# Kernel optimization log

Hardware: AMD Instinct MI355X
Metric: run time of the kernel (lower is better)

## Reference

```python
import jax, jax.numpy as jnp
import numpy as np

DIM = 1024
HEADS = 16
DIM_HEAD = 64
INNER = HEADS * DIM_HEAD  # 1024
SCALE = DIM_HEAD ** -0.5


def setup_inputs() -> dict:
    key = jax.random.key(0)
    k_x, k_qkv, k_out, k_g, k_b = jax.random.split(key, 5)
    x = jax.random.normal(k_x, (4, 2048, DIM), dtype=jnp.float32)
    # LayerNorm affine params (torch default: weight=1, bias=0; keep learnable-shaped)
    ln_gamma = jnp.ones((DIM,), dtype=jnp.float32)
    ln_beta = jnp.zeros((DIM,), dtype=jnp.float32)
    w_qkv = jax.random.normal(k_qkv, (DIM, 3 * INNER), dtype=jnp.float32) * (DIM ** -0.5)
    w_out = jax.random.normal(k_out, (INNER, DIM), dtype=jnp.float32) * (INNER ** -0.5)
    return {"x": x, "ln_gamma": ln_gamma, "ln_beta": ln_beta, "w_qkv": w_qkv, "w_out": w_out}


def reference(x, ln_gamma, ln_beta, w_qkv, w_out):
    # LayerNorm (eps matches torch default 1e-5)
    mu = jnp.mean(x, axis=-1, keepdims=True)
    var = jnp.mean(jnp.square(x - mu), axis=-1, keepdims=True)
    xn = (x - mu) * jax.lax.rsqrt(var + 1e-5) * ln_gamma + ln_beta

    qkv = xn @ w_qkv  # [b, n, 3*inner]
    q, k, v = jnp.split(qkv, 3, axis=-1)

    def to_heads(t):  # b n (h d) -> b h n d
        b, n, _ = t.shape
        return t.reshape(b, n, HEADS, DIM_HEAD).transpose(0, 2, 1, 3)

    q, k, v = to_heads(q), to_heads(k), to_heads(v)

    dots = jnp.einsum('bhid,bhjd->bhij', q, k) * SCALE  # [b,h,n,n]
    attn = jax.nn.softmax(dots, axis=-1)
    out = jnp.einsum('bhij,bhjd->bhid', attn, v)  # [b,h,n,d]

    b, h, n, d = out.shape
    out = out.transpose(0, 2, 1, 3).reshape(b, n, h * d)  # b h n d -> b n (h d)
    return out @ w_out
```

## Files before the change

### kernel.cpp

```cpp
#include <hip/hip_runtime.h>

#define DIM 1024
#define HEADS 16
#define DHEAD 64
#define SEQ 2048
#define BATCH 4
#define ROWS (BATCH*SEQ)
#define QK_COLS (3*DIM)
#define QSCALE 0.18033688011112042f

typedef __bf16 bf16x8 __attribute__((ext_vector_type(8)));
typedef __bf16 bf16x4 __attribute__((ext_vector_type(4)));
typedef short s16x4 __attribute__((ext_vector_type(4)));
typedef float f32x4 __attribute__((ext_vector_type(4)));
typedef unsigned short u16;
typedef unsigned int u32;

__device__ __forceinline__ u16 f2bf(float f) {
  u32 u = __float_as_uint(f);
  u = (u + 0x7fffu + ((u >> 16) & 1u)) >> 16;
  return (u16)u;
}

__device__ __forceinline__ void gld16(const void* g, void* s) {
  __builtin_amdgcn_global_load_lds((__attribute__((address_space(1))) void*)g,
                                   (__attribute__((address_space(3))) void*)s, 16, 0, 0);
}

__device__ __forceinline__ float fexp2(float x) {
#if defined(__HIP_DEVICE_COMPILE__)
  return __builtin_amdgcn_exp2f(x);
#else
  return x;
#endif
}

__device__ __forceinline__ f32x4 mfma16(s16x4 a, s16x4 b, f32x4 c) {
#if defined(__HIP_DEVICE_COMPILE__)
  return __builtin_amdgcn_mfma_f32_16x16x16bf16_1k(a, b, c, 0, 0, 0);
#else
  return c;
#endif
}

__device__ __forceinline__ s16x4 pack_bf16(f32x4 v) {
  bf16x4 b = __builtin_convertvector(v, bf16x4);
  union { bf16x4 b; s16x4 s; } u; u.b = b; return u.s;
}

__global__ __launch_bounds__(256) void ln_kernel(const float* __restrict__ x,
    const float* __restrict__ gam, const float* __restrict__ bet, u16* __restrict__ xn) {
  int row = blockIdx.x, tid = threadIdx.x;
  int lane = tid & 63, w = tid >> 6;
  const float4 xv = *(const float4*)(x + (size_t)row*DIM + tid*4);
  float s = xv.x + xv.y + xv.z + xv.w;
  float q = xv.x*xv.x + xv.y*xv.y + xv.z*xv.z + xv.w*xv.w;
  for (int off = 32; off > 0; off >>= 1) { s += __shfl_xor(s, off, 64); q += __shfl_xor(q, off, 64); }
  __shared__ float red[8];
  if (lane == 0) { red[w] = s; red[4+w] = q; }
  __syncthreads();
  s = red[0]+red[1]+red[2]+red[3];
  q = red[4]+red[5]+red[6]+red[7];
  float mean = s * (1.0f/DIM);
  float rstd = rsqrtf(q*(1.0f/DIM) - mean*mean + 1e-5f);
  float4 gv = *(const float4*)(gam + tid*4);
  float4 bv = *(const float4*)(bet + tid*4);
  ushort4 o;
  o.x = f2bf((xv.x-mean)*rstd*gv.x + bv.x);
  o.y = f2bf((xv.y-mean)*rstd*gv.y + bv.y);
  o.z = f2bf((xv.z-mean)*rstd*gv.z + bv.z);
  o.w = f2bf((xv.w-mean)*rstd*gv.w + bv.w);
  *(ushort4*)(xn + (size_t)row*DIM + tid*4) = o;
}

__global__ __launch_bounds__(256) void transpose_w(const float* __restrict__ in,
    u16* __restrict__ out, int R, int C) {
  __shared__ float tile[32][33];
  int c0 = blockIdx.x * 32, r0 = blockIdx.y * 32;
  int tx = threadIdx.x & 31, ty = threadIdx.x >> 5;
  for (int i = 0; i < 32; i += 8)
    tile[ty+i][tx] = in[(size_t)(r0+ty+i)*C + c0 + tx];
  __syncthreads();
  for (int i = 0; i < 32; i += 8)
    out[(size_t)(c0+ty+i)*R + r0 + tx] = f2bf(tile[tx][ty+i]);
}

template<int NOUT, int EPI>
__global__ __launch_bounds__(256, 2) void gemm_bt(const u16* __restrict__ A, const u16* __restrict__ Bt,
                                                  void* __restrict__ Cv, u16* __restrict__ vT, int K) {
  __shared__ alignas(16) u16 As[128*32];
  __shared__ alignas(16) u16 Bs[128*32];
  int tid = threadIdx.x;
  int lane = tid & 63, w = tid >> 6;
  int l = lane & 15, quad = lane >> 4;
  int wm = (w & 1) * 64, wn = (w >> 1) * 64;
  int m0 = blockIdx.y * 128, n0 = blockIdx.x * 128;
  const u16* Ag = A + (size_t)m0 * K;
  const u16* Bg = Bt + (size_t)n0 * K;
  bool sw = (EPI == 1) || (n0 < 2048);
  f32x4 z = {0.f, 0.f, 0.f, 0.f};
  f32x4 acc[4][4];
  for (int i = 0; i < 4; ++i) for (int j = 0; j < 4; ++j) acc[i][j] = z;
  for (int kt = 0; kt < K; kt += 32) {
    __syncthreads();
    for (int c = 0; c < 2; ++c) {
      int idx = c*256 + tid;
      int row = idx >> 2, col = (idx & 3) << 3;
      gld16(Ag + (size_t)row*K + kt + col, (u16*)As + idx*8);
      gld16(Bg + (size_t)row*K + kt + col, (u16*)Bs + idx*8);
    }
    __syncthreads();
    bf16x8 af[4], bfr[4];
    for (int t = 0; t < 4; ++t) {
      af[t]  = *(const bf16x8*)(As + (wm + t*16 + l)*32 + quad*8);
      bfr[t] = *(const bf16x8*)(Bs + (wn + t*16 + l)*32 + quad*8);
    }
    if (sw) {
      for (int i = 0; i < 4; ++i)
        for (int j = 0; j < 4; ++j)
          acc[i][j] = __builtin_amdgcn_mfma_f32_16x16x32_bf16(bfr[i], af[j], acc[i][j], 0, 0, 0);
    } else {
      for (int i = 0; i < 4; ++i)
        for (int j = 0; j < 4; ++j)
          acc[i][j] = __builtin_amdgcn_mfma_f32_16x16x32_bf16(af[i], bfr[j], acc[i][j], 0, 0, 0);
    }
  }
  if (EPI == 0) {
    u16* C = (u16*)Cv;
    int region = n0 >> 10;
    if (region == 0) {
      for (int i = 0; i < 4; ++i)
        for (int j = 0; j < 4; ++j) {
          int nq = n0 + wn + i*16 + quad*4;
          int m  = m0 + wm + j*16 + l;
          f32x4 v = acc[i][j] * QSCALE;
          *(s16x4*)(C + (size_t)m*QK_COLS + nq) = pack_bf16(v);
        }
    } else if (region == 1) {
      for (int i = 0; i < 4; ++i)
        for (int j = 0; j < 4; ++j) {
          int nq = n0 + wn + i*16 + quad*4;
          int m  = m0 + wm + j*16 + l;
          int d  = nq & 63;
          int col = (nq & ~63) | ((((d >> 3) ^ (m & 7)) << 3) | (d & 7));
          *(s16x4*)(C + (size_t)m*QK_COLS + col) = pack_bf16(acc[i][j]);
        }
    } else {
      for (int i = 0; i < 4; ++i)
        for (int j = 0; j < 4; ++j) {
          int mrow = m0 + wm + i*16 + quad*4;
          int hd   = (n0 - 2048) + wn + j*16 + l;
          int h = hd >> 6, d = hd & 63;
          int bb = mrow >> 11, nloc = mrow & 2047;
          int c = nloc >> 2;
          int cs = (c & ~31) | ((c & 31) ^ (d & 31));
          *(s16x4*)(vT + ((size_t)(bb*16 + h)*DHEAD + d)*SEQ + cs*4) = pack_bf16(acc[i][j]);
        }
    }
  } else {
    float* C = (float*)Cv;
    for (int i = 0; i < 4; ++i)
      for (int j = 0; j < 4; ++j) {
        int n = n0 + wn + i*16 + quad*4;
        int m = m0 + wm + j*16 + l;
        *(f32x4*)(C + (size_t)m*NOUT + n) = acc[i][j];
      }
  }
}

__global__ __launch_bounds__(256, 2) void attn_kernel(const u16* __restrict__ qkv,
    const u16* __restrict__ vT, u16* __restrict__ aout) {
  __shared__ alignas(16) u16 smem[32768];
  int tid = threadIdx.x;
  int lane = tid & 63, w = tid >> 6;
  int l = lane & 15, quad = lane >> 4;
  int bh = blockIdx.x, qt = blockIdx.y;
  int b = bh >> 4, h = bh & 15;
  int qrow0 = b*SEQ + qt*128;

  bf16x8 aq[2][2];
  #pragma unroll
  for (int mt = 0; mt < 2; ++mt)
    #pragma unroll
    for (int ks = 0; ks < 2; ++ks)
      aq[mt][ks] = *(const bf16x8*)(qkv + (size_t)(qrow0 + w*32 + mt*16 + l)*QK_COLS + h*DHEAD + ks*32 + quad*8);

  f32x4 z = {0.f,0.f,0.f,0.f};
  f32x4 o[4][2];
  #pragma unroll
  for (int dt = 0; dt < 4; ++dt) for (int mt = 0; mt < 2; ++mt) o[dt][mt] = z;
  f32x4 psum[2] = {z, z};

  const u16* kbase = qkv + (size_t)b*SEQ*QK_COLS + DIM + h*DHEAD;
  const u16* vbase = vT + (size_t)bh*DHEAD*SEQ;

  #pragma unroll
  for (int c = 0; c < 4; ++c) {
    int idx = c*256 + tid;
    gld16(kbase + (size_t)(idx >> 3)*QK_COLS + ((idx & 7) << 3), smem + idx*8);
    gld16(vbase + (size_t)(idx >> 4)*SEQ + ((idx & 15) << 3), smem + 8192 + idx*8);
  }

  for (int kt = 0; kt < 16; ++kt) {
    __syncthreads();
    const u16* Kt = smem + (kt & 1)*16384;
    const u16* Vt = Kt + 8192;
    if (kt < 15) {
      u16* dst = (u16*)smem + ((kt+1) & 1)*16384;
      int krow0 = (kt+1)*128;
      #pragma unroll
      for (int c = 0; c < 4; ++c) {
        int idx = c*256 + tid;
        gld16(kbase + (size_t)(krow0 + (idx >> 3))*QK_COLS + ((idx & 7) << 3), dst + idx*8);
        gld16(vbase + (size_t)(idx >> 4)*SEQ + krow0 + ((idx & 15) << 3), dst + 8192 + idx*8);
      }
    }

    s16x4 pb[2][8];
    #pragma unroll
    for (int mt = 0; mt < 2; ++mt) {
      f32x4 st[8];
      #pragma unroll
      for (int jt = 0; jt < 8; ++jt) st[jt] = z;
      #pragma unroll
      for (int jt = 0; jt < 8; ++jt) {
        #pragma unroll
        for (int ks = 0; ks < 2; ++ks) {
          bf16x8 bk = *(const bf16x8*)(Kt + (jt*16 + l)*64 + (((ks*4 + quad) ^ (l & 7)) << 3));
          st[jt] = __builtin_amdgcn_mfma_f32_16x16x32_bf16(bk, aq[mt][ks], st[jt], 0,0,0);
        }
      }
      #pragma unroll
      for (int jt = 0; jt < 8; ++jt) {
        f32x4 p;
        p[0] = fexp2(st[jt][0]); p[1] = fexp2(st[jt][1]);
        p[2] = fexp2(st[jt][2]); p[3] = fexp2(st[jt][3]);
        psum[mt] += p;
        pb[mt][jt] = pack_bf16(p);
      }
    }

    #pragma unroll
    for (int jt = 0; jt < 8; ++jt) {
      #pragma unroll
      for (int dt = 0; dt < 4; ++dt) {
        int d = dt*16 + l;
        s16x4 av = *(const s16x4*)(Vt + d*128 + ((((jt*4 + quad) ^ (d & 31)) & 31) << 2));
        o[dt][0] = mfma16(av, pb[0][jt], o[dt][0]);
        o[dt][1] = mfma16(av, pb[1][jt], o[dt][1]);
      }
    }
  }

  float li[2];
  #pragma unroll
  for (int mt = 0; mt < 2; ++mt) {
    float ps = psum[mt][0] + psum[mt][1] + psum[mt][2] + psum[mt][3];
    ps += __shfl_xor(ps, 16, 64);
    ps += __shfl_xor(ps, 32, 64);
    li[mt] = ps;
  }

  __syncthreads();
  u16* Ep = smem + w*2304;
  #pragma unroll
  for (int mt = 0; mt < 2; ++mt) {
    float inv = 1.0f / li[mt];
    #pragma unroll
    for (int dt = 0; dt < 4; ++dt)
      #pragma unroll
      for (int r = 0; r < 4; ++r)
        Ep[(mt*16 + l)*72 + dt*16 + quad*4 + r] = f2bf(o[dt][mt][r] * inv);
  }
  __asm__ volatile("s_waitcnt lgkmcnt(0)" ::: "memory");
  int lr = lane >> 1, half = lane & 1;
  size_t grow = (size_t)qrow0 + w*32 + lr;
  #pragma unroll
  for (int k = 0; k < 4; ++k) {
    uint4 vv = *(const uint4*)(Ep + lr*72 + half*32 + k*8);
    *(uint4*)(aout + grow*DIM + h*DHEAD + half*32 + k*8) = vv;
  }
}

extern "C" void kernel_launch(void* const* d_in, const int* in_sizes, int n_in,
                              void* d_out, int out_size, void* d_ws, size_t ws_size,
                              hipStream_t stream) {
  const float* x    = (const float*)d_in[0];
  const float* gam  = (const float*)d_in[1];
  const float* bet  = (const float*)d_in[2];
  const float* wqkv = (const float*)d_in[3];
  const float* wout = (const float*)d_in[4];
  float* out = (float*)d_out;

  u16* xn    = (u16*)d_ws;
  u16* wqkvT = xn    + (size_t)ROWS*DIM;
  u16* woutT = wqkvT + (size_t)QK_COLS*DIM;
  u16* qkvb  = woutT + (size_t)DIM*DIM;
  u16* vTb   = qkvb  + (size_t)ROWS*QK_COLS;
  u16* aoutb = vTb   + (size_t)64*DHEAD*SEQ;

  ln_kernel<<<ROWS, 256, 0, stream>>>(x, gam, bet, xn);
  transpose_w<<<dim3(QK_COLS/32, DIM/32), 256, 0, stream>>>(wqkv, wqkvT, DIM, QK_COLS);
  transpose_w<<<dim3(DIM/32, DIM/32), 256, 0, stream>>>(wout, woutT, DIM, DIM);
  gemm_bt<QK_COLS,0><<<dim3(QK_COLS/128, ROWS/128), 256, 0, stream>>>(xn, wqkvT, (void*)qkvb, vTb, DIM);
  attn_kernel<<<dim3(64, SEQ/128), 256, 0, stream>>>(qkvb, vTb, aoutb);
  gemm_bt<DIM,1><<<dim3(DIM/128, ROWS/128), 256, 0, stream>>>(aoutb, woutT, (void*)out, nullptr, DIM);
}
```

Baseline: 301.7 us.

## Double-buffer GEMM LDS tiles and merge LayerNorm and weight transposes into one kernel

Merges the LayerNorm kernel and both weight-transpose kernels into a single prep kernel whose blocks branch on block index, removing two launches. The GEMM now uses a double-buffered shared-memory tile: it preloads the first K-tile, then issues loads for the next tile before computing on the current one, which drops one barrier per iteration and lets global loads overlap the MFMA work. Inner loops are also explicitly unrolled. Shared memory per GEMM block doubles to 32 KB, which may limit occupancy, and overlap depends on how gld16 is implemented.

```diff
diff --git a/kernel.cpp b/kernel.cpp
--- a/kernel.cpp
+++ b/kernel.cpp
@@ -48,48 +48,58 @@
   union { bf16x4 b; s16x4 s; } u; u.b = b; return u.s;
 }
 
-__global__ __launch_bounds__(256) void ln_kernel(const float* __restrict__ x,
-    const float* __restrict__ gam, const float* __restrict__ bet, u16* __restrict__ xn) {
-  int row = blockIdx.x, tid = threadIdx.x;
-  int lane = tid & 63, w = tid >> 6;
-  const float4 xv = *(const float4*)(x + (size_t)row*DIM + tid*4);
-  float s = xv.x + xv.y + xv.z + xv.w;
-  float q = xv.x*xv.x + xv.y*xv.y + xv.z*xv.z + xv.w*xv.w;
-  for (int off = 32; off > 0; off >>= 1) { s += __shfl_xor(s, off, 64); q += __shfl_xor(q, off, 64); }
-  __shared__ float red[8];
-  if (lane == 0) { red[w] = s; red[4+w] = q; }
-  __syncthreads();
-  s = red[0]+red[1]+red[2]+red[3];
-  q = red[4]+red[5]+red[6]+red[7];
-  float mean = s * (1.0f/DIM);
-  float rstd = rsqrtf(q*(1.0f/DIM) - mean*mean + 1e-5f);
-  float4 gv = *(const float4*)(gam + tid*4);
-  float4 bv = *(const float4*)(bet + tid*4);
-  ushort4 o;
-  o.x = f2bf((xv.x-mean)*rstd*gv.x + bv.x);
-  o.y = f2bf((xv.y-mean)*rstd*gv.y + bv.y);
-  o.z = f2bf((xv.z-mean)*rstd*gv.z + bv.z);
-  o.w = f2bf((xv.w-mean)*rstd*gv.w + bv.w);
-  *(ushort4*)(xn + (size_t)row*DIM + tid*4) = o;
-}
-
-__global__ __launch_bounds__(256) void transpose_w(const float* __restrict__ in,
-    u16* __restrict__ out, int R, int C) {
+__global__ __launch_bounds__(256) void prep_kernel(
+    const float* __restrict__ x, const float* __restrict__ gam, const float* __restrict__ bet,
+    u16* __restrict__ xn,
+    const float* __restrict__ wqkv, u16* __restrict__ wqkvT,
+    const float* __restrict__ wout, u16* __restrict__ woutT) {
   __shared__ float tile[32][33];
-  int c0 = blockIdx.x * 32, r0 = blockIdx.y * 32;
-  int tx = threadIdx.x & 31, ty = threadIdx.x >> 5;
-  for (int i = 0; i < 32; i += 8)
-    tile[ty+i][tx] = in[(size_t)(r0+ty+i)*C + c0 + tx];
-  __syncthreads();
-  for (int i = 0; i < 32; i += 8)
-    out[(size_t)(c0+ty+i)*R + r0 + tx] = f2bf(tile[tx][ty+i]);
+  int bid = blockIdx.x, tid = threadIdx.x;
+  if (bid < ROWS) {
+    int lane = tid & 63, w = tid >> 6;
+    const float4 xv = *(const float4*)(x + (size_t)bid*DIM + tid*4);
+    float s = xv.x + xv.y + xv.z + xv.w;
+    float q = xv.x*xv.x + xv.y*xv.y + xv.z*xv.z + xv.w*xv.w;
+    for (int off = 32; off > 0; off >>= 1) { s += __shfl_xor(s, off, 64); q += __shfl_xor(q, off, 64); }
+    float* red = &tile[0][0];
+    if (lane == 0) { red[w] = s; red[4+w] = q; }
+    __syncthreads();
+    s = red[0]+red[1]+red[2]+red[3];
+    q = red[4]+red[5]+red[6]+red[7];
+    float mean = s * (1.0f/DIM);
+    float rstd = rsqrtf(q*(1.0f/DIM) - mean*mean + 1e-5f);
+    float4 gv = *(const float4*)(gam + tid*4);
+    float4 bv = *(const float4*)(bet + tid*4);
+    ushort4 o;
+    o.x = f2bf((xv.x-mean)*rstd*gv.x + bv.x);
+    o.y = f2bf((xv.y-mean)*rstd*gv.y + bv.y);
+    o.z = f2bf((xv.z-mean)*rstd*gv.z + bv.z);
+    o.w = f2bf((xv.w-mean)*rstd*gv.w + bv.w);
+    *(ushort4*)(xn + (size_t)bid*DIM + tid*4) = o;
+  } else {
+    const float* in; u16* out; int R, C, c0, r0;
+    if (bid < ROWS + 3072) {
+      int t = bid - ROWS;
+      in = wqkv; out = wqkvT; R = DIM; C = QK_COLS;
+      c0 = (t % 96) * 32; r0 = (t / 96) * 32;
+    } else {
+      int t = bid - ROWS - 3072;
+      in = wout; out = woutT; R = DIM; C = DIM;
+      c0 = (t & 31) * 32; r0 = (t >> 5) * 32;
+    }
+    int tx = tid & 31, ty = tid >> 5;
+    for (int i = 0; i < 32; i += 8)
+      tile[ty+i][tx] = in[(size_t)(r0+ty+i)*C + c0 + tx];
+    __syncthreads();
+    for (int i = 0; i < 32; i += 8)
+      out[(size_t)(c0+ty+i)*R + r0 + tx] = f2bf(tile[tx][ty+i]);
+  }
 }
 
 template<int NOUT, int EPI>
 __global__ __launch_bounds__(256, 2) void gemm_bt(const u16* __restrict__ A, const u16* __restrict__ Bt,
                                                   void* __restrict__ Cv, u16* __restrict__ vT, int K) {
-  __shared__ alignas(16) u16 As[128*32];
-  __shared__ alignas(16) u16 Bs[128*32];
+  __shared__ alignas(16) u16 smem[16384];
   int tid = threadIdx.x;
   int lane = tid & 63, w = tid >> 6;
   int l = lane & 15, quad = lane >> 4;
@@ -101,30 +111,52 @@
   f32x4 z = {0.f, 0.f, 0.f, 0.f};
   f32x4 acc[4][4];
   for (int i = 0; i < 4; ++i) for (int j = 0; j < 4; ++j) acc[i][j] = z;
-  for (int kt = 0; kt < K; kt += 32) {
+
+  #pragma unroll
+  for (int c = 0; c < 2; ++c) {
+    int idx = c*256 + tid;
+    int row = idx >> 2, col = (idx & 3) << 3;
+    gld16(Ag + (size_t)row*K + col, smem + idx*8);
+    gld16(Bg + (size_t)row*K + col, smem + 4096 + idx*8);
+  }
+
+  int NT = K >> 5;
+  for (int kt = 0; kt < NT; ++kt) {
     __syncthreads();
-    for (int c = 0; c < 2; ++c) {
-      int idx = c*256 + tid;
-      int row = idx >> 2, col = (idx & 3) << 3;
-      gld16(Ag + (size_t)row*K + kt + col, (u16*)As + idx*8);
-      gld16(Bg + (size_t)row*K + kt + col, (u16*)Bs + idx*8);
-    }
-    __syncthreads();
+    const u16* As = smem + (kt & 1)*8192;
+    const u16* Bs = As + 4096;
+    if (kt + 1 < NT) {
+      u16* dst = (u16*)smem + ((kt+1) & 1)*8192;
+      int ko = (kt+1)*32;
+      #pragma unroll
+      for (int c = 0; c < 2; ++c) {
+        int idx = c*256 + tid;
+        int row = idx >> 2, col = (idx & 3) << 3;
+        gld16(Ag + (size_t)row*K + ko + col, dst + idx*8);
+        gld16(Bg + (size_t)row*K + ko + col, dst + 4096 + idx*8);
+      }
+    }
     bf16x8 af[4], bfr[4];
+    #pragma unroll
     for (int t = 0; t < 4; ++t) {
       af[t]  = *(const bf16x8*)(As + (wm + t*16 + l)*32 + quad*8);
       bfr[t] = *(const bf16x8*)(Bs + (wn + t*16 + l)*32 + quad*8);
     }
     if (sw) {
-      for (int i = 0; i < 4; ++i)
+      #pragma unroll
+      for (int i = 0; i < 4; ++i)
+        #pragma unroll
         for (int j = 0; j < 4; ++j)
           acc[i][j] = __builtin_amdgcn_mfma_f32_16x16x32_bf16(bfr[i], af[j], acc[i][j], 0, 0, 0);
     } else {
-      for (int i = 0; i < 4; ++i)
+      #pragma unroll
+      for (int i = 0; i < 4; ++i)
+        #pragma unroll
         for (int j = 0; j < 4; ++j)
           acc[i][j] = __builtin_amdgcn_mfma_f32_16x16x32_bf16(af[i], bfr[j], acc[i][j], 0, 0, 0);
     }
   }
+
   if (EPI == 0) {
     u16* C = (u16*)Cv;
     int region = n0 >> 10;
@@ -299,9 +331,7 @@
   u16* vTb   = qkvb  + (size_t)ROWS*QK_COLS;
   u16* aoutb = vTb   + (size_t)64*DHEAD*SEQ;
 
-  ln_kernel<<<ROWS, 256, 0, stream>>>(x, gam, bet, xn);
-  transpose_w<<<dim3(QK_COLS/32, DIM/32), 256, 0, stream>>>(wqkv, wqkvT, DIM, QK_COLS);
-  transpose_w<<<dim3(DIM/32, DIM/32), 256, 0, stream>>>(wout, woutT, DIM, DIM);
+  prep_kernel<<<ROWS + 3072 + 1024, 256, 0, stream>>>(x, gam, bet, xn, wqkv, wqkvT, wout, woutT);
   gemm_bt<QK_COLS,0><<<dim3(QK_COLS/128, ROWS/128), 256, 0, stream>>>(xn, wqkvT, (void*)qkvb, vTb, DIM);
   attn_kernel<<<dim3(64, SEQ/128), 256, 0, stream>>>(qkvb, vTb, aoutb);
   gemm_bt<DIM,1><<<dim3(DIM/128, ROWS/128), 256, 0, stream>>>(aoutb, woutT, (void*)out, nullptr, DIM);
```

Result: faster. 284.7 us (-5.6%).
